# Optimization experiments

Measured on AMD Instinct MI355X. Metric: run time of the kernel, lower is better.

Reference implementation:

```python
import jax, jax.numpy as jnp
import numpy as np

B, S, D, H = 2, 2048, 1024, 16
HD = D // H  # head dim = 64


def setup_inputs() -> dict:
    key = jax.random.key(0)
    ks = jax.random.split(key, 5)
    scale = 1.0 / np.sqrt(D)
    return {
        "hidden_states": jax.random.normal(ks[0], (B, S, D), jnp.float32),
        "attention_mask": jax.random.normal(ks[1], (B, 1, 1, S), jnp.float32),
        "Wq": jax.random.normal(ks[2], (D, D), jnp.float32) * scale,
        "bq": jnp.zeros((D,), jnp.float32),
        "Wk": jax.random.normal(ks[3], (D, D), jnp.float32) * scale,
        "bk": jnp.zeros((D,), jnp.float32),
        "Wv": jax.random.normal(ks[4], (D, D), jnp.float32) * scale,
        "bv": jnp.zeros((D,), jnp.float32),
    }


def _split_heads(x):
    # [B,S,D] -> [B,H,S,HD]
    return x.reshape(B, S, H, HD).transpose(0, 2, 1, 3)


def reference(hidden_states, attention_mask, Wq, bq, Wk, bk, Wv, bv):
    # torch Linear: y = x @ W.T + b
    q = _split_heads(hidden_states @ Wq.T + bq)
    k = _split_heads(hidden_states @ Wk.T + bk)
    v = _split_heads(hidden_states @ Wv.T + bv)

    scores = jnp.einsum("bhqd,bhkd->bhqk", q, k)
    # Faithful to source: with a mask present, the 1/sqrt(head_dim) scaling
    # is overwritten and raw scores are multiplied by the binary key mask.
    mask = (attention_mask >= 0).astype(scores.dtype)  # [B,1,1,S]
    probs = scores * mask
    # dropout prob = 0 (eval) -> identity

    ctx = jnp.einsum("bhqk,bhkd->bhqd", probs, v)
    ctx = ctx.transpose(0, 2, 1, 3).reshape(B, S, D)
    return ctx
```

## Files before the change

kernel.cpp:

```cpp
#include <hip/hip_runtime.h>

#define BB 2
#define SS 2048
#define DD 1024
#define HH 16
#define HDIM 64
#define MTOT 4096

typedef unsigned short u16;
typedef __bf16 bf16_t;
typedef bf16_t bf16x8 __attribute__((ext_vector_type(8)));
typedef float floatx4 __attribute__((ext_vector_type(4)));
typedef float floatx16 __attribute__((ext_vector_type(16)));

__device__ __forceinline__ float bf2f(u16 u) {
  union { unsigned int i; float f; } x;
  x.i = ((unsigned int)u) << 16;
  return x.f;
}
__device__ __forceinline__ u16 f2bf(float f) {
  union { float f; unsigned int i; } x;
  x.f = f;
  unsigned int r = x.i + 0x7fffu + ((x.i >> 16) & 1u);
  return (u16)(r >> 16);
}

__device__ __forceinline__ void gload16(const u16* g, u16* l) {
  __builtin_amdgcn_global_load_lds(
      (const __attribute__((address_space(1))) unsigned int*)g,
      (__attribute__((address_space(3))) unsigned int*)l, 16, 0, 0);
}

__global__ __launch_bounds__(256) void cast_to_bf16(
    const float* __restrict__ hs, const float* __restrict__ wq,
    const float* __restrict__ wk, const float* __restrict__ wv,
    u16* __restrict__ hs_b, u16* __restrict__ wq_b,
    u16* __restrict__ wk_b, u16* __restrict__ wv_b) {
  int fid = blockIdx.x * 256 + threadIdx.x;
  const float* src;
  u16* dst;
  int local;
  if (fid < 1048576) { src = hs; dst = hs_b; local = fid; }
  else if (fid < 1310720) { src = wq; dst = wq_b; local = fid - 1048576; }
  else if (fid < 1572864) { src = wk; dst = wk_b; local = fid - 1310720; }
  else { src = wv; dst = wv_b; local = fid - 1572864; }
  float4 v = reinterpret_cast<const float4*>(src)[local];
  ushort4 o;
  o.x = f2bf(v.x); o.y = f2bf(v.y); o.z = f2bf(v.z); o.w = f2bf(v.w);
  reinterpret_cast<ushort4*>(dst)[local] = o;
}

#define BKK 64
__global__ __launch_bounds__(256) void qkv_gemm_kernel(
    const u16* __restrict__ A,
    const u16* __restrict__ Wq, const u16* __restrict__ Wk, const u16* __restrict__ Wv,
    const float* __restrict__ bq, const float* __restrict__ bk, const float* __restrict__ bv,
    u16* __restrict__ Qo, u16* __restrict__ Ko, u16* __restrict__ Vo) {
  __shared__ u16 sA[128 * BKK];
  __shared__ u16 sB[128 * BKK];
  const int mt = blockIdx.y, ntall = blockIdx.x;
  const int seg = ntall >> 3, nt = ntall & 7;
  const u16* Wp = (seg == 0) ? Wq : (seg == 1) ? Wk : Wv;
  const float* bp = (seg == 0) ? bq : (seg == 1) ? bk : bv;
  u16* Out = (seg == 0) ? Qo : (seg == 1) ? Ko : Vo;
  const int m0 = mt * 128, n0 = nt * 128;
  const int tid = threadIdx.x;
  const int lane = tid & 63, wave = tid >> 6;
  const int wm = (wave >> 1) * 64, wn = (wave & 1) * 64;
  const int l32 = lane & 31, khalf = lane >> 5;
  int srow[4], sgc[4], soff[4];
#pragma unroll
  for (int c = 0; c < 4; ++c) {
    int L = c * 256 + tid;
    srow[c] = L >> 3;
    sgc[c] = ((L & 7) ^ (srow[c] & 7)) << 3;
    soff[c] = L << 3;
  }
  floatx16 acc[2][2] = {};
  for (int k0 = 0; k0 < DD; k0 += BKK) {
#pragma unroll
    for (int c = 0; c < 4; ++c) {
      gload16(A + (size_t)(m0 + srow[c]) * DD + k0 + sgc[c], sA + soff[c]);
      gload16(Wp + (size_t)(n0 + srow[c]) * DD + k0 + sgc[c], sB + soff[c]);
    }
    __syncthreads();
#pragma unroll
    for (int kk = 0; kk < 4; ++kk) {
      const int sw = ((kk * 2 + khalf) ^ (l32 & 7)) << 3;
      bf16x8 af[2], bfr[2];
#pragma unroll
      for (int i = 0; i < 2; ++i)
        af[i] = *reinterpret_cast<const bf16x8*>(sA + (wm + i * 32 + l32) * BKK + sw);
#pragma unroll
      for (int j = 0; j < 2; ++j)
        bfr[j] = *reinterpret_cast<const bf16x8*>(sB + (wn + j * 32 + l32) * BKK + sw);
#pragma unroll
      for (int i = 0; i < 2; ++i)
#pragma unroll
        for (int j = 0; j < 2; ++j)
          acc[i][j] = __builtin_amdgcn_mfma_f32_32x32x16_bf16(af[i], bfr[j], acc[i][j], 0, 0, 0);
    }
    __syncthreads();
  }
#pragma unroll
  for (int j = 0; j < 2; ++j) {
    int col = n0 + wn + j * 32 + l32;
    float bias = bp[col];
#pragma unroll
    for (int i = 0; i < 2; ++i) {
#pragma unroll
      for (int reg = 0; reg < 16; ++reg) {
        int row = m0 + wm + i * 32 + (reg & 3) + 8 * (reg >> 2) + 4 * khalf;
        Out[(size_t)row * DD + col] = f2bf(acc[i][j][reg] + bias);
      }
    }
  }
}

__global__ __launch_bounds__(256) void m_partial_kernel(
    const u16* __restrict__ Xb, const u16* __restrict__ Yb,
    const float* __restrict__ am, float* __restrict__ mpart) {
  __shared__ float sX[64 * 68];
  __shared__ float sY[64 * 68];
  const int bh = blockIdx.y;
  const int b = bh >> 4, h = bh & 15;
  const int tid = threadIdx.x;
  const int e0 = (tid & 15) * 4, d0 = (tid >> 4) * 4;
  float acc[4][4] = {};
  for (int cs = 0; cs < 2; ++cs) {
    const int s0 = (blockIdx.x * 2 + cs) * 64;
    if (cs) __syncthreads();
#pragma unroll
    for (int c = 0; c < 2; ++c) {
      int L = tid + c * 256;
      int srow = L >> 3;
      int col = (L & 7) * 8;
      size_t g = (size_t)(b * SS + s0 + srow) * DD + h * HDIM + col;
      uint4 xraw = *reinterpret_cast<const uint4*>(Xb + g);
      uint4 yraw = *reinterpret_cast<const uint4*>(Yb + g);
      float m = (am[b * SS + s0 + srow] >= 0.f) ? 1.f : 0.f;
      unsigned int xw[4] = {xraw.x, xraw.y, xraw.z, xraw.w};
      unsigned int yw[4] = {yraw.x, yraw.y, yraw.z, yraw.w};
#pragma unroll
      for (int q = 0; q < 4; ++q) {
        sX[srow * 68 + col + 2 * q]     = m * bf2f((u16)(xw[q] & 0xffffu));
        sX[srow * 68 + col + 2 * q + 1] = m * bf2f((u16)(xw[q] >> 16));
        sY[srow * 68 + col + 2 * q]     = bf2f((u16)(yw[q] & 0xffffu));
        sY[srow * 68 + col + 2 * q + 1] = bf2f((u16)(yw[q] >> 16));
      }
    }
    __syncthreads();
    for (int s = 0; s < 64; ++s) {
      float4 xx = *reinterpret_cast<const float4*>(&sX[s * 68 + e0]);
      float4 yy = *reinterpret_cast<const float4*>(&sY[s * 68 + d0]);
      float xa[4] = {xx.x, xx.y, xx.z, xx.w};
      float ya[4] = {yy.x, yy.y, yy.z, yy.w};
#pragma unroll
      for (int i = 0; i < 4; ++i)
#pragma unroll
        for (int j = 0; j < 4; ++j) acc[i][j] += xa[i] * ya[j];
    }
  }
  float* outp = mpart + ((size_t)(blockIdx.x * 32 + bh)) * 4096;
#pragma unroll
  for (int i = 0; i < 4; ++i) {
    float4 o = {acc[i][0], acc[i][1], acc[i][2], acc[i][3]};
    *reinterpret_cast<float4*>(&outp[(e0 + i) * 64 + d0]) = o;
  }
}

__global__ __launch_bounds__(256) void ctx_kernel(
    const u16* __restrict__ Qb, const float* __restrict__ mpart, float* __restrict__ Out) {
  __shared__ u16 sMT[64 * 72];
  const int m0 = blockIdx.x * 128;
  const int h = blockIdx.y;
  const int b = m0 >> 11;
  const int bh = b * HH + h;
  const int tid = threadIdx.x;
#pragma unroll
  for (int c = 0; c < 4; ++c) {
    int L4 = c * 256 + tid;
    float4 s = {0.f, 0.f, 0.f, 0.f};
#pragma unroll
    for (int pc = 0; pc < 16; ++pc) {
      const float4* p4 = reinterpret_cast<const float4*>(mpart + ((size_t)(pc * 32 + bh)) * 4096);
      float4 t = p4[L4];
      s.x += t.x; s.y += t.y; s.z += t.z; s.w += t.w;
    }
    int d = L4 >> 4, e = (L4 & 15) * 4;
    ushort4 o = {f2bf(s.x), f2bf(s.y), f2bf(s.z), f2bf(s.w)};
    *reinterpret_cast<ushort4*>(&sMT[d * 72 + e]) = o;
  }
  __syncthreads();
  const int lane = tid & 63, wave = tid >> 6;
  const int l32 = lane & 31, khalf = lane >> 5;
  const int arow = m0 + wave * 32 + l32;
  const u16* qrow = Qb + (size_t)arow * DD + h * HDIM + khalf * 8;
  bf16x8 af[4], bfr[2][4];
#pragma unroll
  for (int k0 = 0; k0 < 4; ++k0) {
    af[k0] = *reinterpret_cast<const bf16x8*>(qrow + k0 * 16);
#pragma unroll
    for (int j = 0; j < 2; ++j)
      bfr[j][k0] = *reinterpret_cast<const bf16x8*>(
          &sMT[(j * 32 + l32) * 72 + k0 * 16 + khalf * 8]);
  }
  floatx16 acc[2] = {};
#pragma unroll
  for (int j = 0; j < 2; ++j)
#pragma unroll
    for (int k0 = 0; k0 < 4; ++k0)
      acc[j] = __builtin_amdgcn_mfma_f32_32x32x16_bf16(af[k0], bfr[j][k0], acc[j], 0, 0, 0);
#pragma unroll
  for (int j = 0; j < 2; ++j) {
    int col = h * HDIM + j * 32 + l32;
#pragma unroll
    for (int reg = 0; reg < 16; ++reg) {
      int r = m0 + wave * 32 + (reg & 3) + 8 * (reg >> 2) + 4 * khalf;
      Out[(size_t)r * DD + col] = acc[j][reg];
    }
  }
}

extern "C" void kernel_launch(void* const* d_in, const int* in_sizes, int n_in,
                              void* d_out, int out_size, void* d_ws, size_t ws_size,
                              hipStream_t stream) {
  const float* hs = (const float*)d_in[0];
  const float* am = (const float*)d_in[1];
  const float* wq = (const float*)d_in[2];
  const float* bq = (const float*)d_in[3];
  const float* wk = (const float*)d_in[4];
  const float* bk = (const float*)d_in[5];
  const float* wv = (const float*)d_in[6];
  const float* bv = (const float*)d_in[7];
  float* out = (float*)d_out;
  char* ws = (char*)d_ws;

  u16* hs_b = (u16*)(ws);
  u16* wq_b = (u16*)(ws + 8388608);
  u16* wk_b = (u16*)(ws + 10485760);
  u16* wv_b = (u16*)(ws + 12582912);
  u16* q_b  = (u16*)(ws + 14680064);
  u16* k_b  = (u16*)(ws + 23068672);
  u16* v_b  = (u16*)(ws + 31457280);
  float* mpart = (float*)(ws + 39845888);

  cast_to_bf16<<<7168, 256, 0, stream>>>(hs, wq, wk, wv, hs_b, wq_b, wk_b, wv_b);
  qkv_gemm_kernel<<<dim3(24, 32), 256, 0, stream>>>(hs_b, wq_b, wk_b, wv_b,
                                                    bq, bk, bv, q_b, k_b, v_b);
  m_partial_kernel<<<dim3(16, 32), 256, 0, stream>>>(v_b, k_b, am, mpart);
  ctx_kernel<<<dim3(32, 16), 256, 0, stream>>>(q_b, mpart, out);
}
```

Before: 153.5 us.

## Triple-buffer QKV GEMM shared-memory tiles with async prefetch; halve m_partial splits

The QKV projection GEMM now uses BK=32 with three shared-memory buffers. Tiles are prefetched two steps ahead and the code uses vmcnt waits plus a single barrier per step instead of two __syncthreads, so global-to-LDS loads overlap with MFMA work. The XOR swizzle of LDS rows is dropped, which may bring back LDS bank conflicts. Separately, m_partial now processes four sequence chunks per block with half as many blocks, which halves the partial buffers ctx_kernel has to reduce but lowers parallelism.

```diff
diff --git a/kernel.cpp b/kernel.cpp
--- a/kernel.cpp
+++ b/kernel.cpp
@@ -50,14 +50,14 @@
   reinterpret_cast<ushort4*>(dst)[local] = o;
 }
 
-#define BKK 64
+#define BKK 32
 __global__ __launch_bounds__(256) void qkv_gemm_kernel(
     const u16* __restrict__ A,
     const u16* __restrict__ Wq, const u16* __restrict__ Wk, const u16* __restrict__ Wv,
     const float* __restrict__ bq, const float* __restrict__ bk, const float* __restrict__ bv,
     u16* __restrict__ Qo, u16* __restrict__ Ko, u16* __restrict__ Vo) {
-  __shared__ u16 sA[128 * BKK];
-  __shared__ u16 sB[128 * BKK];
+  __shared__ u16 sA[3][128 * BKK];
+  __shared__ u16 sB[3][128 * BKK];
   const int mt = blockIdx.y, ntall = blockIdx.x;
   const int seg = ntall >> 3, nt = ntall & 7;
   const u16* Wp = (seg == 0) ? Wq : (seg == 1) ? Wk : Wv;
@@ -68,40 +68,57 @@
   const int lane = tid & 63, wave = tid >> 6;
   const int wm = (wave >> 1) * 64, wn = (wave & 1) * 64;
   const int l32 = lane & 31, khalf = lane >> 5;
-  int srow[4], sgc[4], soff[4];
-#pragma unroll
-  for (int c = 0; c < 4; ++c) {
-    int L = c * 256 + tid;
-    srow[c] = L >> 3;
-    sgc[c] = ((L & 7) ^ (srow[c] & 7)) << 3;
-    soff[c] = L << 3;
-  }
+  const int srow0 = wave * 32 + (lane >> 2);
+  const int scol = (lane & 3) * 8;
+
+#define STAGE(buf, kbase)                                                    \
+  {                                                                          \
+    _Pragma("unroll") for (int c = 0; c < 2; ++c) {                          \
+      int r = srow0 + c * 16;                                                \
+      gload16(A + (size_t)(m0 + r) * DD + (kbase) + scol,                    \
+              sA[buf] + r * BKK + scol);                                     \
+      gload16(Wp + (size_t)(n0 + r) * DD + (kbase) + scol,                   \
+              sB[buf] + r * BKK + scol);                                     \
+    }                                                                        \
+  }
+
   floatx16 acc[2][2] = {};
-  for (int k0 = 0; k0 < DD; k0 += BKK) {
-#pragma unroll
-    for (int c = 0; c < 4; ++c) {
-      gload16(A + (size_t)(m0 + srow[c]) * DD + k0 + sgc[c], sA + soff[c]);
-      gload16(Wp + (size_t)(n0 + srow[c]) * DD + k0 + sgc[c], sB + soff[c]);
-    }
-    __syncthreads();
-#pragma unroll
-    for (int kk = 0; kk < 4; ++kk) {
-      const int sw = ((kk * 2 + khalf) ^ (l32 & 7)) << 3;
+  STAGE(0, 0);
+  STAGE(1, BKK);
+  asm volatile("s_waitcnt vmcnt(4)" ::: "memory");
+  asm volatile("s_barrier" ::: "memory");
+
+  int cur = 0;
+  for (int t = 0; t < 32; ++t) {
+    if (t < 30) {
+      int nb = cur + 2;
+      if (nb >= 3) nb -= 3;
+      STAGE(nb, (t + 2) * BKK);
+    }
+    const u16* pA = sA[cur];
+    const u16* pB = sB[cur];
+#pragma unroll
+    for (int kk = 0; kk < 2; ++kk) {
       bf16x8 af[2], bfr[2];
 #pragma unroll
       for (int i = 0; i < 2; ++i)
-        af[i] = *reinterpret_cast<const bf16x8*>(sA + (wm + i * 32 + l32) * BKK + sw);
+        af[i] = *reinterpret_cast<const bf16x8*>(pA + (wm + i * 32 + l32) * BKK + kk * 16 + khalf * 8);
 #pragma unroll
       for (int j = 0; j < 2; ++j)
-        bfr[j] = *reinterpret_cast<const bf16x8*>(sB + (wn + j * 32 + l32) * BKK + sw);
+        bfr[j] = *reinterpret_cast<const bf16x8*>(pB + (wn + j * 32 + l32) * BKK + kk * 16 + khalf * 8);
 #pragma unroll
       for (int i = 0; i < 2; ++i)
 #pragma unroll
         for (int j = 0; j < 2; ++j)
           acc[i][j] = __builtin_amdgcn_mfma_f32_32x32x16_bf16(af[i], bfr[j], acc[i][j], 0, 0, 0);
     }
-    __syncthreads();
-  }
+    if (t < 30) asm volatile("s_waitcnt vmcnt(4)" ::: "memory");
+    else if (t == 30) asm volatile("s_waitcnt vmcnt(0)" ::: "memory");
+    if (t < 31) asm volatile("s_barrier" ::: "memory");
+    cur = (cur < 2) ? cur + 1 : 0;
+  }
+#undef STAGE
+
 #pragma unroll
   for (int j = 0; j < 2; ++j) {
     int col = n0 + wn + j * 32 + l32;
@@ -127,8 +144,8 @@
   const int tid = threadIdx.x;
   const int e0 = (tid & 15) * 4, d0 = (tid >> 4) * 4;
   float acc[4][4] = {};
-  for (int cs = 0; cs < 2; ++cs) {
-    const int s0 = (blockIdx.x * 2 + cs) * 64;
+  for (int cs = 0; cs < 4; ++cs) {
+    const int s0 = (blockIdx.x * 4 + cs) * 64;
     if (cs) __syncthreads();
 #pragma unroll
     for (int c = 0; c < 2; ++c) {
@@ -182,7 +199,7 @@
     int L4 = c * 256 + tid;
     float4 s = {0.f, 0.f, 0.f, 0.f};
 #pragma unroll
-    for (int pc = 0; pc < 16; ++pc) {
+    for (int pc = 0; pc < 8; ++pc) {
       const float4* p4 = reinterpret_cast<const float4*>(mpart + ((size_t)(pc * 32 + bh)) * 4096);
       float4 t = p4[L4];
       s.x += t.x; s.y += t.y; s.z += t.z; s.w += t.w;
@@ -248,6 +265,6 @@
   cast_to_bf16<<<7168, 256, 0, stream>>>(hs, wq, wk, wv, hs_b, wq_b, wk_b, wv_b);
   qkv_gemm_kernel<<<dim3(24, 32), 256, 0, stream>>>(hs_b, wq_b, wk_b, wv_b,
                                                     bq, bk, bv, q_b, k_b, v_b);
-  m_partial_kernel<<<dim3(16, 32), 256, 0, stream>>>(v_b, k_b, am, mpart);
+  m_partial_kernel<<<dim3(8, 32), 256, 0, stream>>>(v_b, k_b, am, mpart);
   ctx_kernel<<<dim3(32, 16), 256, 0, stream>>>(q_b, mpart, out);
 }
```

Result: no change. 151.5 us (-1.3%).
